# Kernel tuning notes

Measured on AMD Instinct MI355X. Metric: run time of the kernel, lower is better.

The kernel has to match this reference:

```python
import jax, jax.numpy as jnp
import numpy as np

P = 16      # patch size
D = 768     # d_model
H = 12      # heads
L = 12      # layers
F = 3072    # d_ff
NC = 1000   # num classes
B = 32
IMG = 224
S = (IMG // P) ** 2 + 1  # 197 tokens (CLS + patches)
EPS = 1e-5


def layernorm(x, s, b):
    m = jnp.mean(x, axis=-1, keepdims=True)
    v = jnp.var(x, axis=-1, keepdims=True)
    return (x - m) * jax.lax.rsqrt(v + EPS) * s + b


def setup_inputs() -> dict:
    key = jax.random.key(0)
    ks = jax.random.split(key, 16)
    sd = 0.02
    patch_dim = P * P * 3  # 768
    inp = {
        "img": jax.random.normal(ks[0], (B, 3, IMG, IMG), jnp.float32),
        "proj_w": jax.random.normal(ks[1], (patch_dim, D), jnp.float32) * sd,
        "proj_b": jnp.zeros((D,), jnp.float32),
        "cls_token": jax.random.normal(ks[2], (1, 1, D), jnp.float32) * sd,
        "pos_emb": jax.random.normal(ks[3], (1, S, D), jnp.float32) * sd,
        # stacked per-layer params [L, ...]
        "ln1_s": jnp.ones((L, D), jnp.float32),
        "ln1_b": jnp.zeros((L, D), jnp.float32),
        "wq": jax.random.normal(ks[4], (L, D, D), jnp.float32) * sd,
        "bq": jnp.zeros((L, D), jnp.float32),
        "wk": jax.random.normal(ks[5], (L, D, D), jnp.float32) * sd,
        "bk": jnp.zeros((L, D), jnp.float32),
        "wv": jax.random.normal(ks[6], (L, D, D), jnp.float32) * sd,
        "bv": jnp.zeros((L, D), jnp.float32),
        "wo": jax.random.normal(ks[7], (L, D, D), jnp.float32) * sd,
        "bo": jnp.zeros((L, D), jnp.float32),
        "ln2_s": jnp.ones((L, D), jnp.float32),
        "ln2_b": jnp.zeros((L, D), jnp.float32),
        "w1": jax.random.normal(ks[8], (L, D, F), jnp.float32) * sd,
        "b1": jnp.zeros((L, F), jnp.float32),
        "w2": jax.random.normal(ks[9], (L, F, D), jnp.float32) * sd,
        "b2": jnp.zeros((L, D), jnp.float32),
        "fnorm_s": jnp.ones((D,), jnp.float32),
        "fnorm_b": jnp.zeros((D,), jnp.float32),
        "head_w": jax.random.normal(ks[10], (D, NC), jnp.float32) * sd,
        "head_b": jnp.zeros((NC,), jnp.float32),
    }
    return inp


def vit_forward(img, proj_w, proj_b, cls_token, pos_emb, ln1_s, ln1_b,
                wq, bq, wk, bk, wv, bv, wo, bo, ln2_s, ln2_b,
                w1, b1, w2, b2, fnorm_s, fnorm_b, head_w, head_b):
    b = img.shape[0]
    g = IMG // P
    # rearrange 'b c (h ph) (w pw) -> b (h w) (ph pw c)'
    x = img.reshape(b, 3, g, P, g, P)
    x = x.transpose(0, 2, 4, 3, 5, 1).reshape(b, g * g, P * P * 3)
    x = x @ proj_w + proj_b                      # [b, 196, D]
    cls = jnp.broadcast_to(cls_token, (b, 1, D))
    x = jnp.concatenate([cls, x], axis=1)        # [b, 197, D]
    x = x + pos_emb                              # learnable positional encoding

    dk = D // H
    scale = 1.0 / jnp.sqrt(jnp.float32(dk))

    def layer(x, p):
        (l1s, l1b, Wq, Bq, Wk, Bk, Wv, Bv, Wo, Bo,
         l2s, l2b, W1, B1, W2, B2) = p
        # pre-norm self-attention with residual
        xn = layernorm(x, l1s, l1b)
        q = (xn @ Wq + Bq).reshape(b, S, H, dk)
        k = (xn @ Wk + Bk).reshape(b, S, H, dk)
        v = (xn @ Wv + Bv).reshape(b, S, H, dk)
        scores = jnp.einsum('bqhd,bkhd->bhqk', q, k) * scale
        attn = jax.nn.softmax(scores, axis=-1)
        ao = jnp.einsum('bhqk,bkhd->bqhd', attn, v).reshape(b, S, D)
        x = x + (ao @ Wo + Bo)
        # pre-norm FFN with residual
        xn = layernorm(x, l2s, l2b)
        h = jax.nn.gelu(xn @ W1 + B1, approximate=False)
        x = x + (h @ W2 + B2)
        return x, None

    params = (ln1_s, ln1_b, wq, bq, wk, bk, wv, bv, wo, bo,
              ln2_s, ln2_b, w1, b1, w2, b2)
    x, _ = jax.lax.scan(layer, x, params)
    x = layernorm(x, fnorm_s, fnorm_b)
    cls_out = x[:, 0, :]
    return cls_out @ head_w + head_b             # [b, num_classes]


def reference(img, proj_w, proj_b, cls_token, pos_emb, ln1_s, ln1_b,
              wq, bq, wk, bk, wv, bv, wo, bo, ln2_s, ln2_b,
              w1, b1, w2, b2, fnorm_s, fnorm_b, head_w, head_b):
    return vit_forward(img, proj_w, proj_b, cls_token, pos_emb, ln1_s, ln1_b,
                       wq, bq, wk, bk, wv, bv, wo, bo, ln2_s, ln2_b,
                       w1, b1, w2, b2, fnorm_s, fnorm_b, head_w, head_b)
```

## Files before the change

### kernel.cpp

```cpp
#include <hip/hip_runtime.h>
#include <stdint.h>

typedef __attribute__((ext_vector_type(4))) float  f32x4;
typedef __attribute__((ext_vector_type(8))) _Float16 f16x8;
typedef __attribute__((ext_vector_type(8))) unsigned short u16x8;

__device__ __forceinline__ unsigned short f2h(float f) {
    _Float16 h = (_Float16)f;
    union { _Float16 h; unsigned short u; } cv; cv.h = h; return cv.u;
}

__device__ __forceinline__ f32x4 mfma16(f16x8 a, f16x8 b, f32x4 c) {
    return __builtin_amdgcn_mfma_f32_16x16x32_f16(a, b, c, 0, 0, 0);
}

__device__ __forceinline__ void async16(const unsigned short* g, unsigned short* l) {
    __builtin_amdgcn_global_load_lds(
        (const __attribute__((address_space(1))) unsigned int*)g,
        (__attribute__((address_space(3))) unsigned int*)l,
        16, 0, 0);
}

template<int EPI>
__global__ __launch_bounds__(256, 4)
void gemm_k(const unsigned short* __restrict__ A, const unsigned short* __restrict__ Bw,
            int M, int K, int N,
            float* __restrict__ p0, unsigned short* __restrict__ p1,
            const float* __restrict__ p2, const float* __restrict__ p3,
            unsigned short* __restrict__ p4, unsigned short* __restrict__ p5)
{
    __shared__ unsigned short lA[2][64 * 32];
    __shared__ unsigned short lB[2][128 * 32];
    const int tid  = threadIdx.x;
    const int lane = tid & 63;
    const int wid  = tid >> 6;

    const int gx  = gridDim.x;
    const int nwg = gx * gridDim.y;
    const int lin = blockIdx.y * gx + blockIdx.x;
    const int q = nwg >> 3, r = nwg & 7;
    const int xcd = lin & 7, i = lin >> 3;
    const int wg  = (xcd < r ? xcd * (q + 1) : r * (q + 1) + (xcd - r) * q) + i;
    const int m0 = (wg / gx) * 64;
    const int n0 = (wg % gx) * 128;

    const int colBase = wid * 32;
    const int fr = lane & 15, fg = lane >> 4;

    f32x4 acc[4][2];
#pragma unroll
    for (int a = 0; a < 4; ++a)
#pragma unroll
        for (int b = 0; b < 2; ++b) acc[a][b] = (f32x4){0.f, 0.f, 0.f, 0.f};

    const int nk = K >> 5;

    auto stage = [&](int buf, int kt) {
        const int k0 = kt << 5;
#pragma unroll
        for (int h = 0; h < 3; ++h) {
            const int c = h * 256 + tid;
            const int wbase = h * 256 + wid * 64;
            if (c < 256) {
                const int row = c >> 2, kc = c & 3;
                const int gkc = kc ^ ((row >> 1) & 3);
                int ar = m0 + row; if (ar > M - 1) ar = M - 1;
                async16(A + (size_t)ar * K + k0 + gkc * 8,
                        &lA[buf][(size_t)wbase * 8]);
            } else {
                const int cb = c - 256;
                const int row = cb >> 2, kc = cb & 3;
                const int gkc = kc ^ ((row >> 1) & 3);
                async16(Bw + (size_t)(n0 + row) * K + k0 + gkc * 8,
                        &lB[buf][(size_t)(wbase - 256) * 8]);
            }
        }
    };

    stage(0, 0);
    for (int kt = 0; kt < nk; ++kt) {
        __syncthreads();
        if (kt + 1 < nk) stage((kt + 1) & 1, kt + 1);
        const int buf = kt & 1;
        f16x8 af[4], bfv[2];
#pragma unroll
        for (int mi = 0; mi < 4; ++mi) {
            int row = mi * 16 + fr;
            int swz = fg ^ ((row >> 1) & 3);
            af[mi] = *(const f16x8*)(&lA[buf][row * 32 + (swz << 3)]);
        }
#pragma unroll
        for (int ni = 0; ni < 2; ++ni) {
            int row = colBase + ni * 16 + fr;
            int swz = fg ^ ((row >> 1) & 3);
            bfv[ni] = *(const f16x8*)(&lB[buf][row * 32 + (swz << 3)]);
        }
#pragma unroll
        for (int mi = 0; mi < 4; ++mi)
#pragma unroll
            for (int ni = 0; ni < 2; ++ni)
                acc[mi][ni] = mfma16(af[mi], bfv[ni], acc[mi][ni]);
    }

#pragma unroll
    for (int mi = 0; mi < 4; ++mi) {
#pragma unroll
        for (int ni = 0; ni < 2; ++ni) {
            const int col = n0 + colBase + ni * 16 + fr;
#pragma unroll
            for (int reg = 0; reg < 4; ++reg) {
                const int row = m0 + mi * 16 + fg * 4 + reg;
                if (row >= M) continue;
                const float v = acc[mi][ni][reg];
                if constexpr (EPI == 0) {
                    int mat = col / 768;
                    int w   = col - mat * 768;
                    int h   = w >> 6, d = w & 63;
                    int b   = row / 197, s = row - b * 197;
                    float val = v + p2[col];
                    if (mat == 2) {
                        p5[(((size_t)b * 12 + h) * 64 + d) * 208 + s] = f2h(val);
                    } else {
                        unsigned short* dst = (mat == 0) ? p1 : p4;
                        dst[(((size_t)b * 12 + h) * 197 + s) * 64 + d] = f2h(val);
                    }
                } else if constexpr (EPI == 1 || EPI == 3) {
                    size_t idx = (size_t)row * 768 + col;
                    p0[idx] = p0[idx] + v + p2[col];
                } else if constexpr (EPI == 2) {
                    float val = v + p2[col];
                    float g = 0.5f * val * (1.0f + erff(val * 0.70710678118654752f));
                    p1[(size_t)row * 3072 + col] = f2h(g);
                } else {
                    int b = row / 196, p = row - b * 196;
                    float val = v + p2[col] + p3[(size_t)(1 + p) * 768 + col];
                    p0[((size_t)(b * 197 + 1 + p)) * 768 + col] = val;
                }
            }
        }
    }
}

__global__ __launch_bounds__(256, 4)
void attn_k(const unsigned short* __restrict__ qb, const unsigned short* __restrict__ kb,
            const unsigned short* __restrict__ vt, unsigned short* __restrict__ ao)
{
    __shared__ float sc[32 * 210];
    __shared__ float rinv[32];

    const int qt = blockIdx.x;
    const int bh = blockIdx.y;
    const int b = bh / 12, h = bh - b * 12;
    const unsigned short* qh  = qb + (size_t)bh * 197 * 64;
    const unsigned short* kh  = kb + (size_t)bh * 197 * 64;
    const unsigned short* vth = vt + (size_t)bh * 64 * 208;
    const int tid = threadIdx.x, lane = tid & 63, wid = tid >> 6;
    const int fr = lane & 15, fg = lane >> 4;

    f16x8 qf[2][2];
#pragma unroll
    for (int mi = 0; mi < 2; ++mi)
#pragma unroll
        for (int kc = 0; kc < 2; ++kc) {
            int s = qt * 32 + mi * 16 + fr; if (s > 196) s = 196;
            qf[mi][kc] = *(const f16x8*)(qh + (size_t)s * 64 + kc * 32 + fg * 8);
        }

    for (int nt = wid; nt < 13; nt += 4) {
        f32x4 a0 = (f32x4){0.f,0.f,0.f,0.f}, a1 = a0;
        int rs = nt * 16 + fr; if (rs > 196) rs = 196;
#pragma unroll
        for (int kc = 0; kc < 2; ++kc) {
            f16x8 kf = *(const f16x8*)(kh + (size_t)rs * 64 + kc * 32 + fg * 8);
            a0 = mfma16(qf[0][kc], kf, a0);
            a1 = mfma16(qf[1][kc], kf, a1);
        }
        int ccol = nt * 16 + fr;
        bool valid = (ccol < 197);
#pragma unroll
        for (int reg = 0; reg < 4; ++reg) {
            int mr = fg * 4 + reg;
            sc[mr * 210 + ccol]        = valid ? a0[reg] * 0.125f : -1e30f;
            sc[(16 + mr) * 210 + ccol] = valid ? a1[reg] * 0.125f : -1e30f;
        }
    }
    __syncthreads();

    {
        int row = tid >> 3, j = tid & 7;
        float m = -1e30f;
        for (int c = j; c < 208; c += 8) m = fmaxf(m, sc[row * 210 + c]);
#pragma unroll
        for (int o = 1; o < 8; o <<= 1) m = fmaxf(m, __shfl_xor(m, o));
        float sum = 0.f;
        for (int c = j; c < 208; c += 8) {
            float e = __expf(sc[row * 210 + c] - m);
            sc[row * 210 + c] = e;
            sum += e;
        }
#pragma unroll
        for (int o = 1; o < 8; o <<= 1) sum += __shfl_xor(sum, o);
        if (j == 0) rinv[row] = 1.0f / sum;
    }
    __syncthreads();

    f32x4 o0 = (f32x4){0.f,0.f,0.f,0.f}, o1 = o0;
    const int dbase = wid * 16;
    for (int kt = 0; kt < 7; ++kt) {
        int kb8 = kt * 32 + fg * 8;
        f16x8 pa0, pa1, vf;
        if (kb8 >= 208) {
#pragma unroll
            for (int j = 0; j < 8; ++j) { pa0[j] = (_Float16)0.f; pa1[j] = (_Float16)0.f; vf[j] = (_Float16)0.f; }
        } else {
            const float* pr0 = &sc[fr * 210 + kb8];
            const float* pr1 = &sc[(16 + fr) * 210 + kb8];
#pragma unroll
            for (int j = 0; j < 8; ++j) { pa0[j] = (_Float16)pr0[j]; pa1[j] = (_Float16)pr1[j]; }
            vf = *(const f16x8*)(vth + (size_t)(dbase + fr) * 208 + kb8);
        }
        o0 = mfma16(pa0, vf, o0);
        o1 = mfma16(pa1, vf, o1);
    }
#pragma unroll
    for (int reg = 0; reg < 4; ++reg) {
        int mr0 = fg * 4 + reg, s0 = qt * 32 + mr0;
        if (s0 < 197)
            ao[((size_t)(b * 197 + s0)) * 768 + h * 64 + dbase + fr] = f2h(o0[reg] * rinv[mr0]);
        int mr1 = 16 + fg * 4 + reg, s1 = qt * 32 + mr1;
        if (s1 < 197)
            ao[((size_t)(b * 197 + s1)) * 768 + h * 64 + dbase + fr] = f2h(o1[reg] * rinv[mr1]);
    }
}

__global__ __launch_bounds__(256, 4)
void ln_k(const float* __restrict__ x, const float* __restrict__ gs,
          const float* __restrict__ gb, unsigned short* __restrict__ out)
{
    const int row = blockIdx.x;
    const int tid = threadIdx.x, lane = tid & 63, wid = tid >> 6;
    const float* xr = x + (size_t)row * 768;
    float v0 = xr[tid], v1 = xr[tid + 256], v2 = xr[tid + 512];
    float s = v0 + v1 + v2;
    float q = v0 * v0 + v1 * v1 + v2 * v2;
#pragma unroll
    for (int o = 1; o < 64; o <<= 1) { s += __shfl_xor(s, o); q += __shfl_xor(q, o); }
    __shared__ float ws[4], wq[4];
    if (lane == 0) { ws[wid] = s; wq[wid] = q; }
    __syncthreads();
    s = ws[0] + ws[1] + ws[2] + ws[3];
    q = wq[0] + wq[1] + wq[2] + wq[3];
    const float mean = s * (1.0f / 768.0f);
    const float rstd = rsqrtf(q * (1.0f / 768.0f) - mean * mean + 1e-5f);
    unsigned short* orow = out + (size_t)row * 768;
    orow[tid]       = f2h((v0 - mean) * rstd * gs[tid]       + gb[tid]);
    orow[tid + 256] = f2h((v1 - mean) * rstd * gs[tid + 256] + gb[tid + 256]);
    orow[tid + 512] = f2h((v2 - mean) * rstd * gs[tid + 512] + gb[tid + 512]);
}

__device__ __forceinline__ void convT_dev(const float* __restrict__ src,
                                          unsigned short* __restrict__ dst,
                                          int K, int N, int bx, int by)
{
    __shared__ float t[64][65];
    const int tid = threadIdx.x;
    const int n0 = bx * 64, k0 = by * 64;
    int r = tid >> 4, cq = tid & 15;
#pragma unroll
    for (int i = 0; i < 4; ++i) {
        f32x4 v = *(const f32x4*)(src + (size_t)(k0 + r + i * 16) * N + n0 + cq * 4);
        t[r + i * 16][cq * 4 + 0] = v.x;
        t[r + i * 16][cq * 4 + 1] = v.y;
        t[r + i * 16][cq * 4 + 2] = v.z;
        t[r + i * 16][cq * 4 + 3] = v.w;
    }
    __syncthreads();
    int nl = tid >> 2, kq = tid & 3;
    u16x8 o0, o1;
#pragma unroll
    for (int j = 0; j < 8; ++j) {
        o0[j] = f2h(t[kq * 16 + j][nl]);
        o1[j] = f2h(t[kq * 16 + 8 + j][nl]);
    }
    unsigned short* d = dst + (size_t)(n0 + nl) * K + k0 + kq * 16;
    *(u16x8*)(d)     = o0;
    *(u16x8*)(d + 8) = o1;
}

__global__ __launch_bounds__(256)
void convT_k(const float* __restrict__ src, unsigned short* __restrict__ dst, int K, int N)
{
    convT_dev(src, dst, K, N, blockIdx.x, blockIdx.y);
}

__global__ __launch_bounds__(256)
void prep_k(const float* __restrict__ wq, const float* __restrict__ wk,
            const float* __restrict__ wv, const float* __restrict__ wo,
            const float* __restrict__ w1, const float* __restrict__ w2,
            const float* __restrict__ bq, const float* __restrict__ bk,
            const float* __restrict__ bv,
            unsigned short* __restrict__ wqkvT, unsigned short* __restrict__ woT,
            unsigned short* __restrict__ w1T, unsigned short* __restrict__ w2T,
            float* __restrict__ bqkv)
{
    const int bid = blockIdx.x;
    if (bid == 1728) {
        for (int c = threadIdx.x; c < 2304; c += 256) {
            int m = c / 768, w = c - m * 768;
            bqkv[c] = (m == 0) ? bq[w] : (m == 1 ? bk[w] : bv[w]);
        }
        return;
    }
    const float* src; unsigned short* dst; int K, N, bx, by;
    if (bid < 576) {
        int mat = bid / 144, r = bid - mat * 144;
        K = 768; N = 768; bx = r % 12; by = r / 12;
        if (mat == 0)      { src = wq; dst = wqkvT; }
        else if (mat == 1) { src = wk; dst = wqkvT + 768ull * 768; }
        else if (mat == 2) { src = wv; dst = wqkvT + 1536ull * 768; }
        else               { src = wo; dst = woT; }
    } else if (bid < 1152) {
        int r = bid - 576; K = 768; N = 3072; bx = r % 48; by = r / 48;
        src = w1; dst = w1T;
    } else {
        int r = bid - 1152; K = 3072; N = 768; bx = r % 12; by = r / 12;
        src = w2; dst = w2T;
    }
    convT_dev(src, dst, K, N, bx, by);
}

__global__ __launch_bounds__(256)
void patch_k(const float* __restrict__ img, unsigned short* __restrict__ patches)
{
    const int t = blockIdx.x;
    const int pxy = threadIdx.x;
    const int b = t / 196, pi = t - b * 196;
    const int gy = pi / 14, gx = pi - gy * 14;
    const int py = pxy >> 4, px = pxy & 15;
    const int yy = gy * 16 + py, xx = gx * 16 + px;
    const float* base = img + ((size_t)b * 3 * 224 + yy) * 224 + xx;
    float c0 = base[0];
    float c1 = base[224 * 224];
    float c2 = base[2 * 224 * 224];
    unsigned short* d = patches + (size_t)t * 768 + pxy * 3;
    d[0] = f2h(c0); d[1] = f2h(c1); d[2] = f2h(c2);
}

__global__ void cls_k(const float* __restrict__ cls, const float* __restrict__ pos,
                      float* __restrict__ x)
{
    int c = blockIdx.x * 256 + threadIdx.x;
    int b = blockIdx.y;
    x[((size_t)b * 197) * 768 + c] = cls[c] + pos[c];
}

__global__ __launch_bounds__(256, 4)
void head_k(const float* __restrict__ x, const float* __restrict__ fs, const float* __restrict__ fb,
            const float* __restrict__ hw, const float* __restrict__ hb, float* __restrict__ out)
{
    __shared__ float xn[768];
    __shared__ float ws[4], wq_[4];
    const int b  = blockIdx.y;
    const int n0 = blockIdx.x * 125;
    const int tid = threadIdx.x, lane = tid & 63, wid = tid >> 6;
    const float* xr = x + (size_t)b * 197 * 768;
    float v0 = xr[tid], v1 = xr[tid + 256], v2 = xr[tid + 512];
    float s = v0 + v1 + v2, q = v0 * v0 + v1 * v1 + v2 * v2;
#pragma unroll
    for (int o = 1; o < 64; o <<= 1) { s += __shfl_xor(s, o); q += __shfl_xor(q, o); }
    if (lane == 0) { ws[wid] = s; wq_[wid] = q; }
    __syncthreads();
    s = ws[0] + ws[1] + ws[2] + ws[3];
    q = wq_[0] + wq_[1] + wq_[2] + wq_[3];
    float mean = s * (1.f / 768.f);
    float rstd = rsqrtf(q * (1.f / 768.f) - mean * mean + 1e-5f);
    xn[tid]       = (v0 - mean) * rstd * fs[tid]       + fb[tid];
    xn[tid + 256] = (v1 - mean) * rstd * fs[tid + 256] + fb[tid + 256];
    xn[tid + 512] = (v2 - mean) * rstd * fs[tid + 512] + fb[tid + 512];
    __syncthreads();

    const int nrel = tid >> 1, half = tid & 1;
    const int n = n0 + nrel;
    float acc = 0.f;
    if (nrel < 125) {
        const float* hp = hw + (size_t)(half * 384) * 1000 + n;
        const float* xp = xn + half * 384;
#pragma unroll 4
        for (int k = 0; k < 384; ++k) acc = fmaf(xp[k], hp[(size_t)k * 1000], acc);
    }
    acc += __shfl_xor(acc, 1);
    if (half == 0 && nrel < 125) out[(size_t)b * 1000 + n] = acc + hb[n];
}

extern "C" void kernel_launch(void* const* d_in, const int* in_sizes, int n_in,
                              void* d_out, int out_size, void* d_ws, size_t ws_size,
                              hipStream_t stream)
{
    (void)in_sizes; (void)n_in; (void)out_size; (void)ws_size;
    const float* img    = (const float*)d_in[0];
    const float* proj_w = (const float*)d_in[1];
    const float* proj_b = (const float*)d_in[2];
    const float* cls_t  = (const float*)d_in[3];
    const float* pos    = (const float*)d_in[4];
    const float* ln1_s  = (const float*)d_in[5];
    const float* ln1_b  = (const float*)d_in[6];
    const float* wq     = (const float*)d_in[7];
    const float* bq     = (const float*)d_in[8];
    const float* wk     = (const float*)d_in[9];
    const float* bk     = (const float*)d_in[10];
    const float* wv     = (const float*)d_in[11];
    const float* bv     = (const float*)d_in[12];
    const float* wo     = (const float*)d_in[13];
    const float* bo     = (const float*)d_in[14];
    const float* ln2_s  = (const float*)d_in[15];
    const float* ln2_b  = (const float*)d_in[16];
    const float* w1     = (const float*)d_in[17];
    const float* b1     = (const float*)d_in[18];
    const float* w2     = (const float*)d_in[19];
    const float* b2     = (const float*)d_in[20];
    const float* fs     = (const float*)d_in[21];
    const float* fb     = (const float*)d_in[22];
    const float* hw     = (const float*)d_in[23];
    const float* hb     = (const float*)d_in[24];

    char* ws = (char*)d_ws;
    size_t off = 0;
    auto alloc = [&](size_t bytes) -> char* {
        char* r = ws + off;
        off += (bytes + 255) & ~(size_t)255;
        return r;
    };
    unsigned short* wqkvT = (unsigned short*)alloc(2304ull * 768 * 2);
    unsigned short* woT   = (unsigned short*)alloc(768ull * 768 * 2);
    unsigned short* w1T   = (unsigned short*)alloc(3072ull * 768 * 2);
    unsigned short* w2T   = (unsigned short*)alloc(768ull * 3072 * 2);
    float*          bqkv  = (float*)alloc(2304 * 4);
    unsigned short* projT = (unsigned short*)alloc(768ull * 768 * 2);
    float*          x     = (float*)alloc(6304ull * 768 * 4);
    unsigned short* xn    = (unsigned short*)alloc(6304ull * 768 * 2);
    unsigned short* qbuf  = (unsigned short*)alloc(4841472ull * 2);
    unsigned short* kbuf  = (unsigned short*)alloc(4841472ull * 2);
    unsigned short* vbufT = (unsigned short*)alloc(384ull * 64 * 208 * 2);
    unsigned short* aob   = (unsigned short*)alloc(6304ull * 768 * 2);
    unsigned short* hbuf  = (unsigned short*)alloc(6304ull * 3072 * 2);
    unsigned short* patches = hbuf;

    convT_k<<<dim3(12, 12), 256, 0, stream>>>(proj_w, projT, 768, 768);
    patch_k<<<dim3(6272), 256, 0, stream>>>(img, patches);
    gemm_k<4><<<dim3(6, 98), 256, 0, stream>>>(patches, projT, 6272, 768, 768,
                                               x, nullptr, proj_b, pos, nullptr, nullptr);
    cls_k<<<dim3(3, 32), 256, 0, stream>>>(cls_t, pos, x);

    for (int l = 0; l < 12; ++l) {
        prep_k<<<dim3(1729), 256, 0, stream>>>(
            wq + (size_t)l * 768 * 768, wk + (size_t)l * 768 * 768,
            wv + (size_t)l * 768 * 768, wo + (size_t)l * 768 * 768,
            w1 + (size_t)l * 768 * 3072, w2 + (size_t)l * 3072 * 768,
            bq + l * 768, bk + l * 768, bv + l * 768,
            wqkvT, woT, w1T, w2T, bqkv);

        ln_k<<<dim3(6304), 256, 0, stream>>>(x, ln1_s + l * 768, ln1_b + l * 768, xn);
        gemm_k<0><<<dim3(18, 99), 256, 0, stream>>>(xn, wqkvT, 6304, 768, 2304,
                                                    nullptr, qbuf, bqkv, nullptr, kbuf, vbufT);
        attn_k<<<dim3(7, 384), 256, 0, stream>>>(qbuf, kbuf, vbufT, aob);
        gemm_k<1><<<dim3(6, 99), 256, 0, stream>>>(aob, woT, 6304, 768, 768,
                                                   x, nullptr, bo + l * 768, nullptr, nullptr, nullptr);
        ln_k<<<dim3(6304), 256, 0, stream>>>(x, ln2_s + l * 768, ln2_b + l * 768, xn);
        gemm_k<2><<<dim3(24, 99), 256, 0, stream>>>(xn, w1T, 6304, 768, 3072,
                                                    nullptr, hbuf, b1 + l * 3072, nullptr, nullptr, nullptr);
        gemm_k<3><<<dim3(6, 99), 256, 0, stream>>>(hbuf, w2T, 6304, 3072, 768,
                                                   x, nullptr, b2 + l * 768, nullptr, nullptr, nullptr);
    }

    head_k<<<dim3(8, 32), 256, 0, stream>>>(x, fs, fb, hw, hb, (float*)d_out);
}
```

Before: 3.399 ms.

## Add 128x256-tile triple-buffered GEMM kernel for QKV and FFN1 projections

Adds a new 512-thread GEMM kernel with 128x256 output tiles, a K step of 64, a three-stage LDS ring filled through async global-to-LDS loads, XOR-swizzled LDS layout, and split A-fragment phases with s_setprio around the MFMA bursts. It replaces the 64x128-tile kernel for the QKV and first FFN GEMMs (both with K=768). The goal is more data reuse per tile and better overlap of loads with MFMA work. In exchange it drops to one workgroup per CU with much larger LDS use, and the coarser grid gives fewer workgroups, which risks tail imbalance on the M=6304 problem.

Result: slower. 3.679 ms (+8.2%).

```diff
diff --git a/kernel.cpp b/kernel.cpp
--- a/kernel.cpp
+++ b/kernel.cpp
@@ -19,6 +19,143 @@
         (const __attribute__((address_space(1))) unsigned int*)g,
         (__attribute__((address_space(3))) unsigned int*)l,
         16, 0, 0);
+}
+
+template<int EPI>
+__global__ __launch_bounds__(512, 1)
+void gemm256_k(const unsigned short* __restrict__ A,
+               const unsigned short* __restrict__ Bw,
+               int M, int N,
+               unsigned short* __restrict__ o1, const float* __restrict__ bias,
+               unsigned short* __restrict__ o4, unsigned short* __restrict__ o5)
+{
+    __shared__ unsigned short lds[3][384 * 64];
+    const int tid = threadIdx.x, lane = tid & 63, w = tid >> 6;
+    const int wm = w >> 2, wn = w & 3;
+    const int fr = lane & 15, fg = lane >> 4;
+
+    const int gx  = gridDim.x;
+    const int nwg = gx * gridDim.y;
+    const int lin = blockIdx.y * gx + blockIdx.x;
+    const int q = nwg >> 3, r = nwg & 7;
+    const int xcd = lin & 7, bi = lin >> 3;
+    const int wg  = (xcd < r ? xcd * (q + 1) : r * (q + 1) + (xcd - r) * q) + bi;
+    const int m0 = (wg / gx) * 128;
+    const int n0 = (wg % gx) * 256;
+
+    f32x4 acc[4][4];
+#pragma unroll
+    for (int a = 0; a < 4; ++a)
+#pragma unroll
+        for (int b = 0; b < 4; ++b) acc[a][b] = (f32x4){0.f, 0.f, 0.f, 0.f};
+
+    auto stageU = [&](int buf, int t, int u) {
+#pragma unroll
+        for (int l = 0; l < 2; ++l) {
+            const int c   = l * 512 + tid;
+            const int row = c >> 3, kcl = c & 7;
+            const int kcg = kcl ^ (row & 7);
+            const unsigned short* src;
+            if (u == 0) {
+                int ar = m0 + row; if (ar > M - 1) ar = M - 1;
+                src = A + (size_t)ar * 768 + t * 64 + kcg * 8;
+            } else {
+                src = Bw + (size_t)(n0 + (u - 1) * 128 + row) * 768 + t * 64 + kcg * 8;
+            }
+            async16(src, &lds[buf][(size_t)(u * 1024 + l * 512 + w * 64) * 8]);
+        }
+    };
+    auto rdA = [&](int buf, int mf, int kk) -> f16x8 {
+        int row = wm * 64 + mf * 16 + fr;
+        int pc  = (kk * 4 + fg) ^ (row & 7);
+        return *(const f16x8*)(&lds[buf][row * 64 + pc * 8]);
+    };
+    auto rdB = [&](int buf, int nf, int kk) -> f16x8 {
+        int row = wn * 64 + nf * 16 + fr;
+        int pc  = (kk * 4 + fg) ^ (row & 7);
+        return *(const f16x8*)(&lds[buf][(128 + row) * 64 + pc * 8]);
+    };
+
+    stageU(0, 0, 0); stageU(0, 0, 1); stageU(0, 0, 2);
+    stageU(1, 1, 0); stageU(1, 1, 1); stageU(1, 1, 2);
+    asm volatile("s_waitcnt vmcnt(6)\ns_barrier" ::: "memory");
+
+    for (int t = 0; t < 12; ++t) {
+        const int rb = t % 3, sb = (t + 2) % 3;
+        const bool st = (t + 2 < 12);
+        f16x8 bfr[4][2];
+#pragma unroll
+        for (int nf = 0; nf < 4; ++nf)
+#pragma unroll
+            for (int kk = 0; kk < 2; ++kk) bfr[nf][kk] = rdB(rb, nf, kk);
+        f16x8 afr[2][2];
+#pragma unroll
+        for (int mf = 0; mf < 2; ++mf)
+#pragma unroll
+            for (int kk = 0; kk < 2; ++kk) afr[mf][kk] = rdA(rb, mf, kk);
+        if (st) { stageU(sb, t + 2, 0); stageU(sb, t + 2, 1); }
+        if (t < 10) asm volatile("s_waitcnt vmcnt(6)\ns_barrier" ::: "memory");
+        else        asm volatile("s_waitcnt vmcnt(0)\ns_barrier" ::: "memory");
+        __builtin_amdgcn_s_setprio(1);
+#pragma unroll
+        for (int mf = 0; mf < 2; ++mf)
+#pragma unroll
+            for (int nf = 0; nf < 4; ++nf)
+#pragma unroll
+                for (int kk = 0; kk < 2; ++kk)
+                    acc[mf][nf] = mfma16(afr[mf][kk], bfr[nf][kk], acc[mf][nf]);
+        __builtin_amdgcn_s_setprio(0);
+        asm volatile("s_barrier" ::: "memory");
+#pragma unroll
+        for (int mf = 0; mf < 2; ++mf)
+#pragma unroll
+            for (int kk = 0; kk < 2; ++kk) afr[mf][kk] = rdA(rb, 2 + mf, kk);
+        if (st) stageU(sb, t + 2, 2);
+        if (t < 10) asm volatile("s_waitcnt vmcnt(6)\ns_barrier" ::: "memory");
+        else        asm volatile("s_waitcnt vmcnt(0)\ns_barrier" ::: "memory");
+        __builtin_amdgcn_s_setprio(1);
+#pragma unroll
+        for (int mf = 0; mf < 2; ++mf)
+#pragma unroll
+            for (int nf = 0; nf < 4; ++nf)
+#pragma unroll
+                for (int kk = 0; kk < 2; ++kk)
+                    acc[2 + mf][nf] = mfma16(afr[mf][kk], bfr[nf][kk], acc[2 + mf][nf]);
+        __builtin_amdgcn_s_setprio(0);
+        asm volatile("s_barrier" ::: "memory");
+    }
+
+#pragma unroll
+    for (int mf = 0; mf < 4; ++mf) {
+#pragma unroll
+        for (int nf = 0; nf < 4; ++nf) {
+            const int col = n0 + wn * 64 + nf * 16 + fr;
+#pragma unroll
+            for (int reg = 0; reg < 4; ++reg) {
+                const int row = m0 + wm * 64 + mf * 16 + fg * 4 + reg;
+                if (row >= M) continue;
+                const float v = acc[mf][nf][reg];
+                if constexpr (EPI == 0) {
+                    int mat = col / 768;
+                    int ww  = col - mat * 768;
+                    int h   = ww >> 6, d = ww & 63;
+                    int b   = row / 197, s = row - b * 197;
+                    float val = v + bias[col];
+                    if (mat == 2) {
+                        o5[(((size_t)b * 12 + h) * 64 + d) * 208 + s] = f2h(val);
+                    } else {
+                        unsigned short* dst = (mat == 0) ? o1 : o4;
+                        dst[(((size_t)b * 12 + h) * 197 + s) * 64 + d] = f2h(val);
+                    }
+                } else {
+                    float val = v + bias[col];
+                    float g = 0.5f * val * (1.0f + erff(val * 0.70710678118654752f));
+                    o1[(size_t)row * 3072 + col] = f2h(g);
+                }
+            }
+        }
+    }
+    (void)N;
 }
 
 template<int EPI>
@@ -112,19 +249,7 @@
                 const int row = m0 + mi * 16 + fg * 4 + reg;
                 if (row >= M) continue;
                 const float v = acc[mi][ni][reg];
-                if constexpr (EPI == 0) {
-                    int mat = col / 768;
-                    int w   = col - mat * 768;
-                    int h   = w >> 6, d = w & 63;
-                    int b   = row / 197, s = row - b * 197;
-                    float val = v + p2[col];
-                    if (mat == 2) {
-                        p5[(((size_t)b * 12 + h) * 64 + d) * 208 + s] = f2h(val);
-                    } else {
-                        unsigned short* dst = (mat == 0) ? p1 : p4;
-                        dst[(((size_t)b * 12 + h) * 197 + s) * 64 + d] = f2h(val);
-                    }
-                } else if constexpr (EPI == 1 || EPI == 3) {
+                if constexpr (EPI == 1 || EPI == 3) {
                     size_t idx = (size_t)row * 768 + col;
                     p0[idx] = p0[idx] + v + p2[col];
                 } else if constexpr (EPI == 2) {
@@ -139,6 +264,7 @@
             }
         }
     }
+    (void)p4; (void)p5;
 }
 
 __global__ __launch_bounds__(256, 4)
@@ -460,14 +586,14 @@
             wqkvT, woT, w1T, w2T, bqkv);
 
         ln_k<<<dim3(6304), 256, 0, stream>>>(x, ln1_s + l * 768, ln1_b + l * 768, xn);
-        gemm_k<0><<<dim3(18, 99), 256, 0, stream>>>(xn, wqkvT, 6304, 768, 2304,
-                                                    nullptr, qbuf, bqkv, nullptr, kbuf, vbufT);
+        gemm256_k<0><<<dim3(9, 50), 512, 0, stream>>>(xn, wqkvT, 6304, 2304,
+                                                      qbuf, bqkv, kbuf, vbufT);
         attn_k<<<dim3(7, 384), 256, 0, stream>>>(qbuf, kbuf, vbufT, aob);
         gemm_k<1><<<dim3(6, 99), 256, 0, stream>>>(aob, woT, 6304, 768, 768,
                                                    x, nullptr, bo + l * 768, nullptr, nullptr, nullptr);
         ln_k<<<dim3(6304), 256, 0, stream>>>(x, ln2_s + l * 768, ln2_b + l * 768, xn);
-        gemm_k<2><<<dim3(24, 99), 256, 0, stream>>>(xn, w1T, 6304, 768, 3072,
-                                                    nullptr, hbuf, b1 + l * 3072, nullptr, nullptr, nullptr);
+        gemm256_k<2><<<dim3(12, 50), 512, 0, stream>>>(xn, w1T, 6304, 3072,
+                                                       hbuf, b1 + l * 3072, nullptr, nullptr);
         gemm_k<3><<<dim3(6, 99), 256, 0, stream>>>(hbuf, w2T, 6304, 3072, 768,
                                                    x, nullptr, b2 + l * 768, nullptr, nullptr, nullptr);
     }
```
